# Kernel optimization log

Hardware: AMD Instinct MI355X
Metric: run time of the kernel (lower is better)

The kernel has to match this reference:

```python
import jax, jax.numpy as jnp
import numpy as np

# Module constants from Net.__init__
KS = (3, 8, 2)          # kernel_size per pseudo-coordinate dim
K = KS[0] * KS[1] * KS[2]  # 48 spline weight matrices per layer
DIM = 3
S = 2 ** DIM            # 8 nonzero degree-1 B-spline supports per edge
MAX_RADIUS = 4.5
N, E = 20000, 500000


def _glorot(key, shape):
    fan = shape[-2] + shape[-1]
    return jax.random.normal(key, shape, jnp.float32) * jnp.sqrt(2.0 / fan)


def setup_inputs() -> dict:
    key = jax.random.key(0)
    ks = jax.random.split(key, 12)
    x = jax.random.normal(ks[0], (N, 1), jnp.float32)
    edge_index = jax.random.randint(ks[1], (2, E), 0, N)
    # raw pseudo-coordinates in [0, max_radius); normalized inside reference
    pseudo = jax.random.uniform(ks[2], (E, DIM), jnp.float32) * MAX_RADIUS
    return {
        "x": x,
        "edge_index": edge_index,
        "pseudo": pseudo,
        "W1": _glorot(ks[3], (K, 1, 32)),   "root1": _glorot(ks[4], (1, 32)),   "b1": jnp.zeros((32,), jnp.float32),
        "W2": _glorot(ks[5], (K, 32, 64)),  "root2": _glorot(ks[6], (32, 64)),  "b2": jnp.zeros((64,), jnp.float32),
        "W3": _glorot(ks[7], (K, 64, 128)), "root3": _glorot(ks[8], (64, 128)), "b3": jnp.zeros((128,), jnp.float32),
    }


def spline_basis(u):
    """Degree-1 open B-spline basis. u: [E, DIM] in [0,1].
    Returns basis [E, S] and flat kernel indices kidx [E, S] into the K weights."""
    ks_f = jnp.array(KS, jnp.float32)
    pos = u * (ks_f - 1.0)                      # [E, DIM]
    lo = jnp.floor(pos)
    frac = pos - lo                             # interpolation weight per dim
    lo_i = lo.astype(jnp.int32)
    # all 2^DIM corner offsets
    bits = jnp.array([[(s >> d) & 1 for d in range(DIM)] for s in range(S)], jnp.int32)  # [S, DIM]
    idx = jnp.clip(lo_i[:, None, :] + bits[None, :, :], 0, jnp.array(KS, jnp.int32) - 1)  # [E, S, DIM]
    w = jnp.where(bits[None, :, :] == 1, frac[:, None, :], 1.0 - frac[:, None, :])        # [E, S, DIM]
    basis = jnp.prod(w, axis=-1)                # [E, S]
    strides = jnp.array([KS[1] * KS[2], KS[2], 1], jnp.int32)
    kidx = (idx * strides[None, None, :]).sum(-1)  # [E, S]
    return basis, kidx


def spline_conv(x, src, dst, basis, kidx, W, root, bias):
    """SplineGCN layer: gather source features, weight by spline basis,
    scatter-add into per-(node, kernel) buckets, then contract with the K
    kernel matrices. Equivalent to sum_e basis * (x_src @ W[kidx]) at dst."""
    c_in = x.shape[1]
    contrib = basis[:, :, None] * x[src][:, None, :]          # [E, S, c_in]
    flat = (dst[:, None] * K + kidx).reshape(-1)              # [E*S]
    acc = jax.ops.segment_sum(contrib.reshape(-1, c_in), flat, num_segments=N * K)
    acc = acc.reshape(N, K, c_in)                             # [N, K, c_in]
    return jnp.einsum('nki,kio->no', acc, W) + x @ root + bias


def reference(x, edge_index, pseudo, W1, root1, b1, W2, root2, b2, W3, root3, b3):
    u = jnp.clip(pseudo / MAX_RADIUS, 0.0, 1.0)
    basis, kidx = spline_basis(u)
    src, dst = edge_index[0], edge_index[1]
    h = jax.nn.relu(spline_conv(x, src, dst, basis, kidx, W1, root1, b1))
    h = jax.nn.relu(spline_conv(h, src, dst, basis, kidx, W2, root2, b2))
    h = jax.nn.relu(spline_conv(h, src, dst, basis, kidx, W3, root3, b3))
    return jax.nn.log_softmax(h, axis=-1)
```

## Files before the change

kernel.cpp:

```cpp
#include <hip/hip_runtime.h>
#include <hip/hip_bf16.h>

#define NN_NODES 20000
#define NE_EDGES 500000
#define KTOT 48

typedef __bf16 bf16x8 __attribute__((ext_vector_type(8)));
typedef float f32x4 __attribute__((ext_vector_type(4)));

__device__ inline unsigned short bf16_rne(float x) {
    unsigned int u = __float_as_uint(x);
    u = (u + 0x7fffu + ((u >> 16) & 1u)) >> 16;
    return (unsigned short)u;
}

__global__ void zero_kernel(int* __restrict__ p, int n) {
    int i = blockIdx.x * 256 + threadIdx.x;
    if (i < n) p[i] = 0;
}

__global__ void count_kernel(const int* __restrict__ ei, int* __restrict__ counts) {
    int e = blockIdx.x * 256 + threadIdx.x;
    if (e < NE_EDGES) atomicAdd(&counts[ei[NE_EDGES + e]], 1);
}

__global__ void scan_kernel(const int* __restrict__ counts, int* __restrict__ row_start) {
    __shared__ int part[256];
    const int CH = (NN_NODES + 255) / 256;
    int t = threadIdx.x;
    int begin = t * CH;
    int end = begin + CH;
    if (end > NN_NODES) end = NN_NODES;
    int sum = 0;
    for (int i = begin; i < end && i < NN_NODES; ++i) sum += counts[i];
    part[t] = sum;
    __syncthreads();
    for (int off = 1; off < 256; off <<= 1) {
        int v = (t >= off) ? part[t - off] : 0;
        __syncthreads();
        part[t] += v;
        __syncthreads();
    }
    int run = (t == 0) ? 0 : part[t - 1];
    for (int i = begin; i < end && i < NN_NODES; ++i) {
        row_start[i] = run;
        run += counts[i];
    }
    if (t == 255) row_start[NN_NODES] = part[255];
}

__global__ void fill_kernel(const int* __restrict__ ei, const int* __restrict__ row_start,
                            int* __restrict__ cursor, int* __restrict__ slot_pos) {
    int e = blockIdx.x * 256 + threadIdx.x;
    if (e < NE_EDGES) {
        int d = ei[NE_EDGES + e];
        int p = atomicAdd(&cursor[d], 1);
        slot_pos[e] = row_start[d] + p;
    }
}

__global__ void edge_prep_sorted(const float* __restrict__ pseudo, const int* __restrict__ ei,
                                 const int* __restrict__ slot_pos,
                                 int* __restrict__ srcs,
                                 float* __restrict__ bas8, unsigned char* __restrict__ kidb) {
    int e = blockIdx.x * 256 + threadIdx.x;
    if (e >= NE_EDGES) return;
    const int ksa[3] = {3, 8, 2};
    float frac[3];
    int id_lo[3], id_hi[3];
#pragma unroll
    for (int d = 0; d < 3; ++d) {
        float u = pseudo[e * 3 + d] * (1.0f / 4.5f);
        u = fminf(fmaxf(u, 0.0f), 1.0f);
        float pos = u * (float)(ksa[d] - 1);
        float fl = floorf(pos);
        int lo = (int)fl;
        frac[d] = pos - fl;
        id_lo[d] = lo;
        id_hi[d] = (lo + 1 <= ksa[d] - 1) ? lo + 1 : lo - 1;
    }
    int j = slot_pos[e];
    srcs[j] = ei[e];
#pragma unroll
    for (int s = 0; s < 8; ++s) {
        float w = 1.0f;
        int k = 0;
        const int strides[3] = {16, 2, 1};
#pragma unroll
        for (int d = 0; d < 3; ++d) {
            int bit = (s >> d) & 1;
            k += (bit ? id_hi[d] : id_lo[d]) * strides[d];
            w *= bit ? frac[d] : (1.0f - frac[d]);
        }
        bas8[(size_t)j * 8 + s] = w;
        kidb[(size_t)j * 8 + s] = (unsigned char)k;
    }
}

__global__ __launch_bounds__(256) void layer1_fused_kernel(
    const int* __restrict__ srcs, const float* __restrict__ bas8,
    const unsigned char* __restrict__ kidb, const int* __restrict__ row_start,
    const float* __restrict__ x, const float* __restrict__ W1,
    const float* __restrict__ root1, const float* __restrict__ b1,
    unsigned short* __restrict__ h1bf) {
    __shared__ float w1s[KTOT * 32];
    __shared__ float scopy[4][8 * 49];
    int tid = threadIdx.x;
    for (int l = tid; l < KTOT * 32; l += 256) w1s[l] = W1[l];
    int w = tid >> 6, lane = tid & 63;
    int n = blockIdx.x * 4 + w;
    bool act = n < NN_NODES;
    float* sc = &scopy[w][0];
    for (int l = lane; l < 8 * 49; l += 64) sc[l] = 0.0f;
    if (act) {
        int beg = row_start[n], end = row_start[n + 1];
        int es = lane >> 3;
        for (int jb = beg; jb < end; jb += 8) {
            int j = jb + es;
            if (j < end) {
                float b = bas8[(size_t)jb * 8 + lane];
                int k = kidb[(size_t)jb * 8 + lane];
                float xv = x[srcs[j]];
                sc[es * 49 + k] += b * xv;
            }
        }
        if (lane < KTOT) {
            float a = 0.0f;
#pragma unroll
            for (int e = 0; e < 8; ++e) a += sc[e * 49 + lane];
            sc[lane] = a;
        }
    }
    __syncthreads();
    if (act && lane < 32) {
        float s = b1[lane] + x[n] * root1[lane];
#pragma unroll 8
        for (int k = 0; k < KTOT; ++k) s = fmaf(sc[k], w1s[k * 32 + lane], s);
        h1bf[n * 32 + lane] = bf16_rne(fmaxf(s, 0.0f));
    }
}

#define BTSTRIDE 40
template <int CIN>
__global__ __launch_bounds__(256) void mfma_acc_kernel(
    const int* __restrict__ srcs, const float* __restrict__ bas8,
    const unsigned char* __restrict__ kidb, const int* __restrict__ row_start,
    const unsigned short* __restrict__ hbf, unsigned short* __restrict__ abuf,
    int n0, int mc) {
    constexpr int NT = CIN / 16;
    __shared__ unsigned short BtAll[4][KTOT * BTSTRIDE];
    int w = threadIdx.x >> 6, lane = threadIdx.x & 63;
    int n_local = blockIdx.x * 4 + w;
    if (n_local >= mc) return;
    int n = n0 + n_local;
    unsigned short* Bt = &BtAll[w][0];
    int q = lane >> 4;
    int l15 = lane & 15;
    int beg = row_start[n], end = row_start[n + 1];
    int cnt = end - beg;
    f32x4 acc[3][NT] = {};

    for (int c0 = 0; c0 < cnt; c0 += 32) {
        uint4 z = make_uint4(0, 0, 0, 0);
        for (int l = lane; l < (KTOT * BTSTRIDE) / 8; l += 64) ((uint4*)Bt)[l] = z;
#pragma unroll
        for (int it = 0; it < 4; ++it) {
            int idx = it * 64 + lane;
            int jj = idx >> 3, s = idx & 7;
            int j = c0 + jj;
            if (j < cnt) {
                float b = bas8[(size_t)(beg + j) * 8 + s];
                int k = kidb[(size_t)(beg + j) * 8 + s];
                Bt[k * BTSTRIDE + jj] = bf16_rne(b);
            }
        }
        int srcv[8];
#pragma unroll
        for (int j = 0; j < 8; ++j) {
            int jc = c0 + q * 8 + j;
            jc = (jc < cnt) ? jc : (cnt - 1);
            srcv[j] = srcs[beg + jc];
        }
        bf16x8 afr[3];
#pragma unroll
        for (int mt = 0; mt < 3; ++mt) {
            uint4 raw = *(const uint4*)&Bt[(mt * 16 + l15) * BTSTRIDE + q * 8];
            afr[mt] = __builtin_bit_cast(bf16x8, raw);
        }
#pragma unroll
        for (int nt = 0; nt < NT; ++nt) {
            unsigned int bw[4];
#pragma unroll
            for (int jp = 0; jp < 4; ++jp) {
                unsigned int lo = hbf[(size_t)srcv[2 * jp] * CIN + nt * 16 + l15];
                unsigned int hi = hbf[(size_t)srcv[2 * jp + 1] * CIN + nt * 16 + l15];
                bw[jp] = lo | (hi << 16);
            }
            uint4 braw = make_uint4(bw[0], bw[1], bw[2], bw[3]);
            bf16x8 bfr = __builtin_bit_cast(bf16x8, braw);
#pragma unroll
            for (int mt = 0; mt < 3; ++mt)
                acc[mt][nt] = __builtin_amdgcn_mfma_f32_16x16x32_bf16(afr[mt], bfr,
                                                                      acc[mt][nt], 0, 0, 0);
        }
    }

    unsigned short* arow = abuf + (size_t)n_local * (49 * CIN);
#pragma unroll
    for (int mt = 0; mt < 3; ++mt)
#pragma unroll
        for (int nt = 0; nt < NT; ++nt)
#pragma unroll
            for (int r = 0; r < 4; ++r) {
                int kk = mt * 16 + q * 4 + r;
                int ch = nt * 16 + l15;
                arow[kk * CIN + ch] = bf16_rne(acc[mt][nt][r]);
            }
    if (lane < CIN) arow[KTOT * CIN + lane] = hbf[(size_t)n * CIN + lane];
}

__global__ void pack_w_kernel(const float* __restrict__ W, const float* __restrict__ root,
                              int KK, int NN, int total, unsigned short* __restrict__ Wp) {
    int tid = blockIdx.x * 256 + threadIdx.x;
    if (tid >= total) return;
    int nct = NN >> 4;
    int l = tid & 63;
    int c = (tid >> 6) % nct;
    int t = tid / (64 * nct);
    int n = c * 16 + (l & 15);
    int kbase = t * 32 + ((l >> 4) << 3);
    unsigned short vals[8];
#pragma unroll
    for (int jj = 0; jj < 8; ++jj) {
        int k = kbase + jj;
        float v = (k < KK) ? W[(size_t)k * NN + n] : root[(size_t)(k - KK) * NN + n];
        vals[jj] = bf16_rne(v);
    }
    *(uint4*)&Wp[(size_t)tid * 8] = *(uint4*)vals;
}

template <int NCT, bool LOGSOFTMAX>
__global__ __launch_bounds__(256) void mfma_gemm_block(
    const unsigned short* __restrict__ A, const unsigned short* __restrict__ Wp,
    const float* __restrict__ bias, void* __restrict__ outp,
    int Kp, int n0, int mc) {
    constexpr int NN = NCT * 16;
    constexpr int RSTR = NN + 2;
    __shared__ float red[4][16 * RSTR];
    int w = threadIdx.x >> 6, lane = threadIdx.x & 63;
    int q = lane >> 4, l15 = lane & 15;
    int row_local = blockIdx.x * 16 + l15;
    int row_c = min(row_local, mc - 1);
    const unsigned short* arow = A + (size_t)row_c * Kp + (q << 3);
    const uint4* wpq = (const uint4*)Wp;
    f32x4 acc[NCT] = {};
    int tsteps = Kp >> 5;
    int t0 = (w * tsteps) >> 2;
    int t1 = ((w + 1) * tsteps) >> 2;

    uint4 na = *(const uint4*)(arow + t0 * 32);
    uint4 nb[NCT];
    {
        const uint4* bb = wpq + ((size_t)t0 * NCT) * 64 + lane;
#pragma unroll
        for (int c = 0; c < NCT; ++c) nb[c] = bb[c * 64];
    }
    for (int t = t0; t < t1; ++t) {
        uint4 ca = na;
        uint4 cb[NCT];
#pragma unroll
        for (int c = 0; c < NCT; ++c) cb[c] = nb[c];
        int tn = (t + 1 < t1) ? t + 1 : t;
        na = *(const uint4*)(arow + tn * 32);
        const uint4* bb = wpq + ((size_t)tn * NCT) * 64 + lane;
#pragma unroll
        for (int c = 0; c < NCT; ++c) nb[c] = bb[c * 64];
        bf16x8 af = __builtin_bit_cast(bf16x8, ca);
#pragma unroll
        for (int c = 0; c < NCT; ++c) {
            bf16x8 bfr = __builtin_bit_cast(bf16x8, cb[c]);
            acc[c] = __builtin_amdgcn_mfma_f32_16x16x32_bf16(af, bfr, acc[c], 0, 0, 0);
        }
    }

    float* myred = &red[w][0];
#pragma unroll
    for (int c = 0; c < NCT; ++c)
#pragma unroll
        for (int r = 0; r < 4; ++r)
            myred[(q * 4 + r) * RSTR + c * 16 + l15] = acc[c][r];
    __syncthreads();

    if (!LOGSOFTMAX) {
        unsigned short* outb = (unsigned short*)outp;
        for (int l = threadIdx.x; l < 16 * NN; l += 256) {
            int row = l / NN, col = l % NN;
            int idx = row * RSTR + col;
            float v = red[0][idx] + red[1][idx] + red[2][idx] + red[3][idx];
            v = fmaxf(v + bias[col], 0.0f);
            int ro = blockIdx.x * 16 + row;
            if (ro < mc) outb[(size_t)(n0 + ro) * NN + col] = bf16_rne(v);
        }
    } else {
        float* outf = (float*)outp;
        int row = threadIdx.x >> 4;
        int cb0 = threadIdx.x & 15;
        float v[8];
        float mx = -1e30f;
#pragma unroll
        for (int c = 0; c < 8; ++c) {
            int col = cb0 + c * 16;
            int idx = row * RSTR + col;
            float s = red[0][idx] + red[1][idx] + red[2][idx] + red[3][idx];
            s = fmaxf(s + bias[col], 0.0f);
            v[c] = s;
            mx = fmaxf(mx, s);
        }
#pragma unroll
        for (int off = 8; off > 0; off >>= 1) mx = fmaxf(mx, __shfl_xor(mx, off));
        float se = 0.0f;
#pragma unroll
        for (int c = 0; c < 8; ++c) se += expf(v[c] - mx);
#pragma unroll
        for (int off = 8; off > 0; off >>= 1) se += __shfl_xor(se, off);
        float lse = mx + logf(se);
        int ro = blockIdx.x * 16 + row;
        if (ro < mc) {
#pragma unroll
            for (int c = 0; c < 8; ++c)
                outf[(size_t)(n0 + ro) * 128 + cb0 + c * 16] = v[c] - lse;
        }
    }
}

extern "C" void kernel_launch(void* const* d_in, const int* in_sizes, int n_in,
                              void* d_out, int out_size, void* d_ws, size_t ws_size,
                              hipStream_t stream) {
    const float* x = (const float*)d_in[0];
    const int* ei = (const int*)d_in[1];
    const float* pseudo = (const float*)d_in[2];
    const float* W1 = (const float*)d_in[3];
    const float* root1 = (const float*)d_in[4];
    const float* b1 = (const float*)d_in[5];
    const float* W2 = (const float*)d_in[6];
    const float* root2 = (const float*)d_in[7];
    const float* b2 = (const float*)d_in[8];
    const float* W3 = (const float*)d_in[9];
    const float* root3 = (const float*)d_in[10];
    const float* b3 = (const float*)d_in[11];
    float* out = (float*)d_out;
    char* ws = (char*)d_ws;

    const int N = NN_NODES, E = NE_EDGES;
    const int Kp2 = 49 * 32;
    const int Kp3 = 49 * 64;
    size_t off = 0;
    auto carve = [&](size_t bytes) {
        size_t p = off;
        off += (bytes + 255) & ~(size_t)255;
        return p;
    };
    int* counts = (int*)(ws + carve((size_t)N * 4 * 2));
    int* cursor = counts + N;
    int* row_start = (int*)(ws + carve((size_t)(N + 1) * 4));
    int* slot_pos = (int*)(ws + carve((size_t)E * 4));
    int* srcs = (int*)(ws + carve((size_t)E * 4));
    float* bas8 = (float*)(ws + carve((size_t)E * 8 * 4));
    unsigned char* kidb = (unsigned char*)(ws + carve((size_t)E * 8));
    unsigned short* h1bf = (unsigned short*)(ws + carve((size_t)N * 32 * 2));
    unsigned short* h2bf = (unsigned short*)(ws + carve((size_t)N * 64 * 2));
    unsigned short* Wp2 = (unsigned short*)(ws + carve((size_t)Kp2 * 64 * 2));
    unsigned short* Wp3 = (unsigned short*)(ws + carve((size_t)Kp3 * 128 * 2));
    size_t rem = (ws_size > off) ? (ws_size - off) : 0;
    unsigned short* abuf = (unsigned short*)(ws + off);

    int ch2 = (int)(rem / ((size_t)Kp2 * 2));
    int ch3 = (int)(rem / ((size_t)Kp3 * 2));
    if (ch2 > N) ch2 = N;
    if (ch3 > N) ch3 = N;
    if (ch2 < 1) ch2 = 1;
    if (ch3 < 1) ch3 = 1;

    int egrid = (E + 255) / 256;

    zero_kernel<<<(2 * N + 255) / 256, 256, 0, stream>>>(counts, 2 * N);
    count_kernel<<<egrid, 256, 0, stream>>>(ei, counts);
    scan_kernel<<<1, 256, 0, stream>>>(counts, row_start);
    fill_kernel<<<egrid, 256, 0, stream>>>(ei, row_start, cursor, slot_pos);
    edge_prep_sorted<<<egrid, 256, 0, stream>>>(pseudo, ei, slot_pos, srcs, bas8, kidb);

    int tot2 = (Kp2 / 32) * (64 / 16) * 64;
    int tot3 = (Kp3 / 32) * (128 / 16) * 64;
    pack_w_kernel<<<(tot2 + 255) / 256, 256, 0, stream>>>(W2, root2, KTOT * 32, 64, tot2, Wp2);
    pack_w_kernel<<<(tot3 + 255) / 256, 256, 0, stream>>>(W3, root3, KTOT * 64, 128, tot3, Wp3);

    layer1_fused_kernel<<<(N + 3) / 4, 256, 0, stream>>>(srcs, bas8, kidb, row_start, x,
                                                         W1, root1, b1, h1bf);

    for (int n0 = 0; n0 < N; n0 += ch2) {
        int mc = N - n0 < ch2 ? N - n0 : ch2;
        mfma_acc_kernel<32><<<(mc + 3) / 4, 256, 0, stream>>>(
            srcs, bas8, kidb, row_start, h1bf, abuf, n0, mc);
        mfma_gemm_block<4, false><<<(mc + 15) / 16, 256, 0, stream>>>(
            abuf, Wp2, b2, h2bf, Kp2, n0, mc);
    }

    for (int n0 = 0; n0 < N; n0 += ch3) {
        int mc = N - n0 < ch3 ? N - n0 : ch3;
        mfma_acc_kernel<64><<<(mc + 3) / 4, 256, 0, stream>>>(
            srcs, bas8, kidb, row_start, h2bf, abuf, n0, mc);
        mfma_gemm_block<8, true><<<(mc + 15) / 16, 256, 0, stream>>>(
            abuf, Wp3, b3, out, Kp3, n0, mc);
    }
}
```

Baseline: 347.0 us.

## Fuse per-node spline accumulation with weight GEMM via shared-memory A rows

Merges the per-node MFMA accumulation kernel and the block GEMM into one kernel per layer. Each wave builds its node's 49*CIN accumulated row in LDS, and after a barrier each wave computes a 16-column output slice over the block's NW nodes. This removes the large global abuf round trip and the extra launches. In exchange, MFMA rows are underused (only NW of 16 rows are distinct nodes), LDS use rises, and each block rereads the full packed weight matrix.

```diff
diff --git a/kernel.cpp b/kernel.cpp
--- a/kernel.cpp
+++ b/kernel.cpp
@@ -4,6 +4,7 @@
 #define NN_NODES 20000
 #define NE_EDGES 500000
 #define KTOT 48
+#define BTSTRIDE 40
 
 typedef __bf16 bf16x8 __attribute__((ext_vector_type(8)));
 typedef float f32x4 __attribute__((ext_vector_type(4)));
@@ -140,85 +141,6 @@
     }
 }
 
-#define BTSTRIDE 40
-template <int CIN>
-__global__ __launch_bounds__(256) void mfma_acc_kernel(
-    const int* __restrict__ srcs, const float* __restrict__ bas8,
-    const unsigned char* __restrict__ kidb, const int* __restrict__ row_start,
-    const unsigned short* __restrict__ hbf, unsigned short* __restrict__ abuf,
-    int n0, int mc) {
-    constexpr int NT = CIN / 16;
-    __shared__ unsigned short BtAll[4][KTOT * BTSTRIDE];
-    int w = threadIdx.x >> 6, lane = threadIdx.x & 63;
-    int n_local = blockIdx.x * 4 + w;
-    if (n_local >= mc) return;
-    int n = n0 + n_local;
-    unsigned short* Bt = &BtAll[w][0];
-    int q = lane >> 4;
-    int l15 = lane & 15;
-    int beg = row_start[n], end = row_start[n + 1];
-    int cnt = end - beg;
-    f32x4 acc[3][NT] = {};
-
-    for (int c0 = 0; c0 < cnt; c0 += 32) {
-        uint4 z = make_uint4(0, 0, 0, 0);
-        for (int l = lane; l < (KTOT * BTSTRIDE) / 8; l += 64) ((uint4*)Bt)[l] = z;
-#pragma unroll
-        for (int it = 0; it < 4; ++it) {
-            int idx = it * 64 + lane;
-            int jj = idx >> 3, s = idx & 7;
-            int j = c0 + jj;
-            if (j < cnt) {
-                float b = bas8[(size_t)(beg + j) * 8 + s];
-                int k = kidb[(size_t)(beg + j) * 8 + s];
-                Bt[k * BTSTRIDE + jj] = bf16_rne(b);
-            }
-        }
-        int srcv[8];
-#pragma unroll
-        for (int j = 0; j < 8; ++j) {
-            int jc = c0 + q * 8 + j;
-            jc = (jc < cnt) ? jc : (cnt - 1);
-            srcv[j] = srcs[beg + jc];
-        }
-        bf16x8 afr[3];
-#pragma unroll
-        for (int mt = 0; mt < 3; ++mt) {
-            uint4 raw = *(const uint4*)&Bt[(mt * 16 + l15) * BTSTRIDE + q * 8];
-            afr[mt] = __builtin_bit_cast(bf16x8, raw);
-        }
-#pragma unroll
-        for (int nt = 0; nt < NT; ++nt) {
-            unsigned int bw[4];
-#pragma unroll
-            for (int jp = 0; jp < 4; ++jp) {
-                unsigned int lo = hbf[(size_t)srcv[2 * jp] * CIN + nt * 16 + l15];
-                unsigned int hi = hbf[(size_t)srcv[2 * jp + 1] * CIN + nt * 16 + l15];
-                bw[jp] = lo | (hi << 16);
-            }
-            uint4 braw = make_uint4(bw[0], bw[1], bw[2], bw[3]);
-            bf16x8 bfr = __builtin_bit_cast(bf16x8, braw);
-#pragma unroll
-            for (int mt = 0; mt < 3; ++mt)
-                acc[mt][nt] = __builtin_amdgcn_mfma_f32_16x16x32_bf16(afr[mt], bfr,
-                                                                      acc[mt][nt], 0, 0, 0);
-        }
-    }
-
-    unsigned short* arow = abuf + (size_t)n_local * (49 * CIN);
-#pragma unroll
-    for (int mt = 0; mt < 3; ++mt)
-#pragma unroll
-        for (int nt = 0; nt < NT; ++nt)
-#pragma unroll
-            for (int r = 0; r < 4; ++r) {
-                int kk = mt * 16 + q * 4 + r;
-                int ch = nt * 16 + l15;
-                arow[kk * CIN + ch] = bf16_rne(acc[mt][nt][r]);
-            }
-    if (lane < CIN) arow[KTOT * CIN + lane] = hbf[(size_t)n * CIN + lane];
-}
-
 __global__ void pack_w_kernel(const float* __restrict__ W, const float* __restrict__ root,
                               int KK, int NN, int total, unsigned short* __restrict__ Wp) {
     int tid = blockIdx.x * 256 + threadIdx.x;
@@ -239,96 +161,143 @@
     *(uint4*)&Wp[(size_t)tid * 8] = *(uint4*)vals;
 }
 
-template <int NCT, bool LOGSOFTMAX>
-__global__ __launch_bounds__(256) void mfma_gemm_block(
-    const unsigned short* __restrict__ A, const unsigned short* __restrict__ Wp,
-    const float* __restrict__ bias, void* __restrict__ outp,
-    int Kp, int n0, int mc) {
-    constexpr int NN = NCT * 16;
-    constexpr int RSTR = NN + 2;
-    __shared__ float red[4][16 * RSTR];
+template <int CIN, int NW, bool LOGSOFTMAX>
+__global__ __launch_bounds__(NW * 64) void fused_layer_kernel(
+    const int* __restrict__ srcs, const float* __restrict__ bas8,
+    const unsigned char* __restrict__ kidb, const int* __restrict__ row_start,
+    const unsigned short* __restrict__ hbf, const unsigned short* __restrict__ Wp,
+    const float* __restrict__ bias, void* __restrict__ outp) {
+    constexpr int NT = CIN / 16;
+    constexpr int KP = 49 * CIN;
+    constexpr int ASTR = KP + 8;
+    constexpr int TSTEPS = KP / 32;
+    __shared__ unsigned short Arows[NW * ASTR];
+    __shared__ unsigned short BtAll[NW][KTOT * BTSTRIDE];
+    float* Cst = (float*)&BtAll[0][0];
     int w = threadIdx.x >> 6, lane = threadIdx.x & 63;
     int q = lane >> 4, l15 = lane & 15;
-    int row_local = blockIdx.x * 16 + l15;
-    int row_c = min(row_local, mc - 1);
-    const unsigned short* arow = A + (size_t)row_c * Kp + (q << 3);
+    unsigned short* Bt = &BtAll[w][0];
+
+    {
+        int n = blockIdx.x * NW + w;
+        int beg = row_start[n], end = row_start[n + 1];
+        int cnt = end - beg;
+        f32x4 acc[3][NT] = {};
+        for (int c0 = 0; c0 < cnt; c0 += 32) {
+            uint4 z = make_uint4(0, 0, 0, 0);
+            for (int l = lane; l < (KTOT * BTSTRIDE) / 8; l += 64) ((uint4*)Bt)[l] = z;
+#pragma unroll
+            for (int it = 0; it < 4; ++it) {
+                int idx = it * 64 + lane;
+                int jj = idx >> 3, s = idx & 7;
+                int j = c0 + jj;
+                if (j < cnt) {
+                    float b = bas8[(size_t)(beg + j) * 8 + s];
+                    int k = kidb[(size_t)(beg + j) * 8 + s];
+                    Bt[k * BTSTRIDE + jj] = bf16_rne(b);
+                }
+            }
+            int srcv[8];
+#pragma unroll
+            for (int j = 0; j < 8; ++j) {
+                int jc = c0 + q * 8 + j;
+                jc = (jc < cnt) ? jc : (cnt - 1);
+                srcv[j] = srcs[beg + jc];
+            }
+            bf16x8 afr[3];
+#pragma unroll
+            for (int mt = 0; mt < 3; ++mt) {
+                uint4 raw = *(const uint4*)&Bt[(mt * 16 + l15) * BTSTRIDE + q * 8];
+                afr[mt] = __builtin_bit_cast(bf16x8, raw);
+            }
+#pragma unroll
+            for (int nt = 0; nt < NT; ++nt) {
+                unsigned int bw[4];
+#pragma unroll
+                for (int jp = 0; jp < 4; ++jp) {
+                    unsigned int lo = hbf[(size_t)srcv[2 * jp] * CIN + nt * 16 + l15];
+                    unsigned int hi = hbf[(size_t)srcv[2 * jp + 1] * CIN + nt * 16 + l15];
+                    bw[jp] = lo | (hi << 16);
+                }
+                uint4 braw = make_uint4(bw[0], bw[1], bw[2], bw[3]);
+                bf16x8 bfr = __builtin_bit_cast(bf16x8, braw);
+#pragma unroll
+                for (int mt = 0; mt < 3; ++mt)
+                    acc[mt][nt] = __builtin_amdgcn_mfma_f32_16x16x32_bf16(
+                        afr[mt], bfr, acc[mt][nt], 0, 0, 0);
+            }
+        }
+        unsigned short* arow = &Arows[w * ASTR];
+#pragma unroll
+        for (int mt = 0; mt < 3; ++mt)
+#pragma unroll
+            for (int nt = 0; nt < NT; ++nt)
+#pragma unroll
+                for (int r = 0; r < 4; ++r)
+                    arow[(mt * 16 + q * 4 + r) * CIN + nt * 16 + l15] =
+                        bf16_rne(acc[mt][nt][r]);
+        if (lane < CIN) arow[KTOT * CIN + lane] = hbf[(size_t)n * CIN + lane];
+    }
+    __syncthreads();
+
+    f32x4 cacc = {};
     const uint4* wpq = (const uint4*)Wp;
-    f32x4 acc[NCT] = {};
-    int tsteps = Kp >> 5;
-    int t0 = (w * tsteps) >> 2;
-    int t1 = ((w + 1) * tsteps) >> 2;
-
-    uint4 na = *(const uint4*)(arow + t0 * 32);
-    uint4 nb[NCT];
-    {
-        const uint4* bb = wpq + ((size_t)t0 * NCT) * 64 + lane;
-#pragma unroll
-        for (int c = 0; c < NCT; ++c) nb[c] = bb[c * 64];
-    }
-    for (int t = t0; t < t1; ++t) {
-        uint4 ca = na;
-        uint4 cb[NCT];
-#pragma unroll
-        for (int c = 0; c < NCT; ++c) cb[c] = nb[c];
-        int tn = (t + 1 < t1) ? t + 1 : t;
-        na = *(const uint4*)(arow + tn * 32);
-        const uint4* bb = wpq + ((size_t)tn * NCT) * 64 + lane;
-#pragma unroll
-        for (int c = 0; c < NCT; ++c) nb[c] = bb[c * 64];
-        bf16x8 af = __builtin_bit_cast(bf16x8, ca);
-#pragma unroll
-        for (int c = 0; c < NCT; ++c) {
-            bf16x8 bfr = __builtin_bit_cast(bf16x8, cb[c]);
-            acc[c] = __builtin_amdgcn_mfma_f32_16x16x32_bf16(af, bfr, acc[c], 0, 0, 0);
-        }
-    }
-
-    float* myred = &red[w][0];
-#pragma unroll
-    for (int c = 0; c < NCT; ++c)
-#pragma unroll
-        for (int r = 0; r < 4; ++r)
-            myred[(q * 4 + r) * RSTR + c * 16 + l15] = acc[c][r];
-    __syncthreads();
+    uint4 nb = wpq[(size_t)w * 64 + lane];
+    int slot = l15 & (NW - 1);
+    for (int t = 0; t < TSTEPS; ++t) {
+        uint4 cb = nb;
+        int tn = (t + 1 < TSTEPS) ? t + 1 : t;
+        nb = wpq[((size_t)tn * NW + w) * 64 + lane];
+        bf16x8 af = __builtin_bit_cast(
+            bf16x8, *(const uint4*)&Arows[slot * ASTR + t * 32 + (q << 3)]);
+        bf16x8 bfr = __builtin_bit_cast(bf16x8, cb);
+        cacc = __builtin_amdgcn_mfma_f32_16x16x32_bf16(af, bfr, cacc, 0, 0, 0);
+    }
 
     if (!LOGSOFTMAX) {
-        unsigned short* outb = (unsigned short*)outp;
-        for (int l = threadIdx.x; l < 16 * NN; l += 256) {
-            int row = l / NN, col = l % NN;
-            int idx = row * RSTR + col;
-            float v = red[0][idx] + red[1][idx] + red[2][idx] + red[3][idx];
-            v = fmaxf(v + bias[col], 0.0f);
-            int ro = blockIdx.x * 16 + row;
-            if (ro < mc) outb[(size_t)(n0 + ro) * NN + col] = bf16_rne(v);
+        if (q == 0) {
+            unsigned short* outb = (unsigned short*)outp;
+            int col = w * 16 + l15;
+            float bv = bias[col];
+#pragma unroll
+            for (int r = 0; r < 4; ++r) {
+                int node = blockIdx.x * NW + r;
+                float v = fmaxf(cacc[r] + bv, 0.0f);
+                outb[(size_t)node * (NW * 16) + col] = bf16_rne(v);
+            }
         }
     } else {
-        float* outf = (float*)outp;
-        int row = threadIdx.x >> 4;
-        int cb0 = threadIdx.x & 15;
-        float v[8];
-        float mx = -1e30f;
-#pragma unroll
-        for (int c = 0; c < 8; ++c) {
-            int col = cb0 + c * 16;
-            int idx = row * RSTR + col;
-            float s = red[0][idx] + red[1][idx] + red[2][idx] + red[3][idx];
-            s = fmaxf(s + bias[col], 0.0f);
-            v[c] = s;
-            mx = fmaxf(mx, s);
-        }
-#pragma unroll
-        for (int off = 8; off > 0; off >>= 1) mx = fmaxf(mx, __shfl_xor(mx, off));
-        float se = 0.0f;
-#pragma unroll
-        for (int c = 0; c < 8; ++c) se += expf(v[c] - mx);
-#pragma unroll
-        for (int off = 8; off > 0; off >>= 1) se += __shfl_xor(se, off);
-        float lse = mx + logf(se);
-        int ro = blockIdx.x * 16 + row;
-        if (ro < mc) {
+        if (q < 2) {
+#pragma unroll
+            for (int r = 0; r < 4; ++r)
+                Cst[(q * 4 + r) * 130 + w * 16 + l15] = cacc[r];
+        }
+        __syncthreads();
+        if (threadIdx.x < 128) {
+            float* outf = (float*)outp;
+            int row = threadIdx.x >> 4;
+            int cb0 = threadIdx.x & 15;
+            float v[8];
+            float mx = -1e30f;
+#pragma unroll
+            for (int c = 0; c < 8; ++c) {
+                float s = Cst[row * 130 + cb0 + c * 16] + bias[cb0 + c * 16];
+                s = fmaxf(s, 0.0f);
+                v[c] = s;
+                mx = fmaxf(mx, s);
+            }
+#pragma unroll
+            for (int off = 8; off > 0; off >>= 1) mx = fmaxf(mx, __shfl_xor(mx, off));
+            float se = 0.0f;
+#pragma unroll
+            for (int c = 0; c < 8; ++c) se += expf(v[c] - mx);
+#pragma unroll
+            for (int off = 8; off > 0; off >>= 1) se += __shfl_xor(se, off);
+            float lse = mx + logf(se);
+            int n = blockIdx.x * NW + row;
 #pragma unroll
             for (int c = 0; c < 8; ++c)
-                outf[(size_t)(n0 + ro) * 128 + cb0 + c * 16] = v[c] - lse;
+                outf[(size_t)n * 128 + cb0 + c * 16] = v[c] - lse;
         }
     }
 }
@@ -371,15 +340,6 @@
     unsigned short* h2bf = (unsigned short*)(ws + carve((size_t)N * 64 * 2));
     unsigned short* Wp2 = (unsigned short*)(ws + carve((size_t)Kp2 * 64 * 2));
     unsigned short* Wp3 = (unsigned short*)(ws + carve((size_t)Kp3 * 128 * 2));
-    size_t rem = (ws_size > off) ? (ws_size - off) : 0;
-    unsigned short* abuf = (unsigned short*)(ws + off);
-
-    int ch2 = (int)(rem / ((size_t)Kp2 * 2));
-    int ch3 = (int)(rem / ((size_t)Kp3 * 2));
-    if (ch2 > N) ch2 = N;
-    if (ch3 > N) ch3 = N;
-    if (ch2 < 1) ch2 = 1;
-    if (ch3 < 1) ch3 = 1;
 
     int egrid = (E + 255) / 256;
 
@@ -397,19 +357,9 @@
     layer1_fused_kernel<<<(N + 3) / 4, 256, 0, stream>>>(srcs, bas8, kidb, row_start, x,
                                                          W1, root1, b1, h1bf);
 
-    for (int n0 = 0; n0 < N; n0 += ch2) {
-        int mc = N - n0 < ch2 ? N - n0 : ch2;
-        mfma_acc_kernel<32><<<(mc + 3) / 4, 256, 0, stream>>>(
-            srcs, bas8, kidb, row_start, h1bf, abuf, n0, mc);
-        mfma_gemm_block<4, false><<<(mc + 15) / 16, 256, 0, stream>>>(
-            abuf, Wp2, b2, h2bf, Kp2, n0, mc);
-    }
-
-    for (int n0 = 0; n0 < N; n0 += ch3) {
-        int mc = N - n0 < ch3 ? N - n0 : ch3;
-        mfma_acc_kernel<64><<<(mc + 3) / 4, 256, 0, stream>>>(
-            srcs, bas8, kidb, row_start, h2bf, abuf, n0, mc);
-        mfma_gemm_block<8, true><<<(mc + 15) / 16, 256, 0, stream>>>(
-            abuf, Wp3, b3, out, Kp3, n0, mc);
-    }
-}
+    fused_layer_kernel<32, 4, false><<<N / 4, 256, 0, stream>>>(
+        srcs, bas8, kidb, row_start, h1bf, Wp2, b2, h2bf);
+
+    fused_layer_kernel<64, 8, true><<<N / 8, 512, 0, stream>>>(
+        srcs, bas8, kidb, row_start, h2bf, Wp3, b3, out);
+}
```

Result: faster. 340.1 us (-2.0%).
